# Kernel tuning notes

Measured on AMD Instinct MI355X. Metric: run time of the kernel, lower is better.

## Reference

```python
import jax, jax.numpy as jnp
import numpy as np

B, T, H, V, E = 128, 256, 512, 50000, 300
FORGET_BIAS = 1.0


def setup_inputs() -> dict:
    key = jax.random.key(0)
    ks = jax.random.split(key, 8)
    s = 0.05
    return {
        "x": jax.random.randint(ks[0], (B, T), 0, V, dtype=jnp.int64),
        "embedding": jax.random.normal(ks[1], (V, E), dtype=jnp.float32),
        "W0": jax.random.normal(ks[2], (E + H, 4 * H), dtype=jnp.float32) * s,
        "b0": jnp.zeros((4 * H,), dtype=jnp.float32),
        "W1": jax.random.normal(ks[3], (2 * H, 4 * H), dtype=jnp.float32) * s,
        "b1": jnp.zeros((4 * H,), dtype=jnp.float32),
        "Wd": jax.random.normal(ks[4], (H, 2), dtype=jnp.float32) * s,
        "bd": jnp.zeros((2,), dtype=jnp.float32),
    }


def _lstm_cell(x, c, h, W, b):
    # TF BasicLSTMCell: gates in i, j, f, o order; forget_bias added to f.
    g = jnp.dot(jnp.concatenate([x, h], axis=1), W) + b  # [B, 4H]
    i, j, f, o = jnp.split(g, 4, axis=1)
    c_new = c * jax.nn.sigmoid(f + FORGET_BIAS) + jax.nn.sigmoid(i) * jnp.tanh(j)
    h_new = jnp.tanh(c_new) * jax.nn.sigmoid(o)
    return c_new, h_new


def reference(x, embedding, W0, b0, W1, b1, Wd, bd):
    vecs = embedding[x]                      # [B, T, E] (frozen embedding lookup)
    vecs_t = jnp.transpose(vecs, (1, 0, 2))  # [T, B, E]

    def step(carry, xt):
        c0, h0, c1, h1 = carry
        c0, h0 = _lstm_cell(xt, c0, h0, W0, b0)
        c1, h1 = _lstm_cell(h0, c1, h1, W1, b1)
        return (c0, h0, c1, h1), None

    z = jnp.zeros((x.shape[0], W0.shape[1] // 4), dtype=embedding.dtype)
    (c0, h0, c1, h1), _ = jax.lax.scan(step, (z, z, z, z), vecs_t)
    logits = jnp.dot(h1, Wd) + bd            # [B, 2]
    return logits
```

## Files before the change

### kernel.cpp

```cpp
#include <hip/hip_runtime.h>

#define Tt 256

#define FLAGS_SHORTS 16384
#define H0OFF  16384
#define H1OFF  (H0OFF + 2*64*128*8)
#define HPAR   (64*128*8)

typedef _Float16 h8 __attribute__((ext_vector_type(8)));
typedef float    f4 __attribute__((ext_vector_type(4)));
typedef unsigned long long ull;
typedef unsigned short u16;

#define MFMA __builtin_amdgcn_mfma_f32_16x16x32_f16
#define LOSC (1.0f/1024.0f)

__device__ inline u16 h_bits(float f){ union{_Float16 h; u16 s;} u; u.h=(_Float16)f; return u.s; }
__device__ inline float bits_f(u16 s){ union{u16 s2; _Float16 h;} u; u.s2=s; return (float)u.h; }
__device__ inline float sigm(float x){ return 1.f/(1.f+expf(-x)); }

__device__ inline __amdgpu_buffer_rsrc_t make_rsrc(const void* base){
    return __builtin_amdgcn_make_buffer_rsrc((void*)base, (short)0,
                                             0xFFFFFFFFu,
                                             0x00020000);
}
__device__ inline h8 ldH(__amdgpu_buffer_rsrc_t rsrc, int u16idx){
    auto d = __builtin_amdgcn_raw_buffer_load_b128(rsrc, u16idx * 2, 0, 17 );
    h8 v; __builtin_memcpy(&v, &d, 16);
    return v;
}

__device__ inline void barrier_arrive(int* __restrict__ flags, int tid, int bid, int target) {
    __builtin_amdgcn_s_waitcnt(0);
    __syncthreads();
    if (tid == 0)
        __hip_atomic_store(flags + bid, target, __ATOMIC_RELAXED, __HIP_MEMORY_SCOPE_AGENT);
}
__device__ inline void barrier_wait(int* __restrict__ flags, int tid, int target) {
    if (tid < 256)
        while (__hip_atomic_load(flags + tid, __ATOMIC_RELAXED, __HIP_MEMORY_SCOPE_AGENT) < target)
            __builtin_amdgcn_s_sleep(4);
    __syncthreads();
}

struct X4 { f4 h0, l0, h1, l1; };

__global__ __launch_bounds__(1024, 1) void lstm_coop(
    const int* __restrict__ x, const float* __restrict__ emb,
    const float* __restrict__ W0, const float* __restrict__ b0,
    const float* __restrict__ W1, const float* __restrict__ b1,
    const float* __restrict__ Wd, const float* __restrict__ bd,
    float* __restrict__ out, u16* __restrict__ ws) {

    const int tid  = threadIdx.x;
    const int lane = tid & 63;
    const int wave = tid >> 6;
    const int mt   = wave & 3;
    const int g4   = wave >> 2;
    const int quad = lane >> 4;
    const int fm   = lane & 15;
    const int bid  = blockIdx.x;
    const int lyr  = bid & 1;
    const int inner= bid >> 1;
    const int bq   = inner >> 6;
    const int cg   = inner & 63;

    __shared__ u16   whi[128 * 32 * 8];
    __shared__ u16   wlo[128 * 32 * 8];
    __shared__ float csm[2][64 * 33];

    int* flags = (int*)ws;
    const __amdgpu_buffer_rsrc_t rsrc = make_rsrc(ws);

    if (lyr == 0) {
        for (int i = tid; i < 104 * 32 * 8; i += 1024) {
            int kg = i >> 8; int rem = i & 255; int n = rem >> 3; int j = rem & 7;
            int k = kg * 8 + j;
            int col = ((n >> 3) << 9) + (cg << 3) + (n & 7);
            float w = 0.f;
            if (k < 300) w = W0[k * 2048 + col];
            else if (k >= 320) w = W0[(k - 20) * 2048 + col];
            _Float16 wh = (_Float16)w;
            union{_Float16 h; u16 s;} uh; uh.h = wh;
            whi[i] = uh.s;
            wlo[i] = h_bits((w - (float)wh) * 1024.0f);
        }
    } else {
        for (int i = tid; i < 128 * 32 * 8; i += 1024) {
            int kg = i >> 8; int rem = i & 255; int n = rem >> 3; int j = rem & 7;
            int k = kg * 8 + j;
            int col = ((n >> 3) << 9) + (cg << 3) + (n & 7);
            float w = W1[k * 2048 + col];
            _Float16 wh = (_Float16)w;
            union{_Float16 h; u16 s;} uh; uh.h = wh;
            whi[i] = uh.s;
            wlo[i] = h_bits((w - (float)wh) * 1024.0f);
        }
    }

    if (tid < 256) {
        int row = bq * 64 + (tid >> 2);
        int c = (tid & 3) << 1;
        unsigned int* pz = (unsigned int*)(ws + (lyr ? H1OFF + 1 * HPAR : H0OFF + 0 * HPAR)
                                           + cg * 1024 + row * 8 + c);
        __hip_atomic_store(pz, 0u, __ATOMIC_RELAXED, __HIP_MEMORY_SCOPE_AGENT);
    }

    const int arow = bq * 64 + mt * 16 + fm;
    const int actm   = tid >> 3;
    const int acthc  = tid & 7;
    const int actrow = bq * 64 + actm;
    const int ca = (cg << 3) + acthc;

    const float bi = lyr ? b1[ca]        : b0[ca];
    const float bj = lyr ? b1[512 + ca]  : b0[512 + ca];
    const float bf = lyr ? b1[1024 + ca] : b0[1024 + ca];
    const float bo = lyr ? b1[1536 + ca] : b0[1536 + ca];

    float cs = 0.f;

    auto xgemm = [&](int pp) -> X4 {
        X4 a; a.h0 = (f4){0,0,0,0}; a.l0 = a.h0; a.h1 = a.h0; a.l1 = a.h0;
        int xi = x[arow * Tt + pp];
        xi = (xi < 0) ? 0 : ((xi >= 50000) ? 49999 : xi);
        const float* embrow = emb + (size_t)xi * 300;
#pragma unroll
        for (int ktl = 0; ktl < 3; ktl++) {
            int kt = ktl * 4 + g4;
            if (kt < 10) {
                int kbase = kt * 32 + quad * 8;
                h8 af;
                if (kt < 9) {
                    f4 u0 = *(const f4*)(embrow + kbase);
                    f4 u1 = *(const f4*)(embrow + kbase + 4);
#pragma unroll
                    for (int e = 0; e < 4; e++) { af[e] = (_Float16)u0[e]; af[4+e] = (_Float16)u1[e]; }
                } else {
#pragma unroll
                    for (int e = 0; e < 8; e++) { int kk = kbase + e; af[e] = (_Float16)((kk < 300) ? embrow[kk] : 0.f); }
                }
                int kb = (kt * 4 + quad) * 32;
                a.h0 = MFMA(af, *(const h8*)&whi[(kb + fm) * 8],      a.h0, 0,0,0);
                a.l0 = MFMA(af, *(const h8*)&wlo[(kb + fm) * 8],      a.l0, 0,0,0);
                a.h1 = MFMA(af, *(const h8*)&whi[(kb + 16 + fm) * 8], a.h1, 0,0,0);
                a.l1 = MFMA(af, *(const h8*)&wlo[(kb + 16 + fm) * 8], a.l1, 0,0,0);
            }
        }
        return a;
    };

    auto reduce_store = [&](const f4& aH0, const f4& aL0, const f4& aH1, const f4& aL1){
        if (g4 < 2) {
#pragma unroll
            for (int r = 0; r < 4; r++) {
                csm[g4][(mt * 16 + quad * 4 + r) * 33 + fm]      = aH0[r] + aL0[r] * LOSC;
                csm[g4][(mt * 16 + quad * 4 + r) * 33 + 16 + fm] = aH1[r] + aL1[r] * LOSC;
            }
        }
        __syncthreads();
        if (g4 >= 2) {
#pragma unroll
            for (int r = 0; r < 4; r++) {
                csm[g4 - 2][(mt * 16 + quad * 4 + r) * 33 + fm]      += aH0[r] + aL0[r] * LOSC;
                csm[g4 - 2][(mt * 16 + quad * 4 + r) * 33 + 16 + fm] += aH1[r] + aL1[r] * LOSC;
            }
        }
        __syncthreads();
    };

    X4 accx;
    barrier_arrive(flags, tid, bid, 1);
    if (lyr == 0) accx = xgemm(0);
    barrier_wait(flags, tid, 1);

    for (int p = 0; p <= Tt; ++p) {
        const int par = p & 1, wpar = 1 - par;

        if (lyr == 1) {
            if (p >= 1) {
                f4 aH0 = (f4){0,0,0,0}, aL0 = aH0, aH1 = aH0, aL1 = aH0;
                const int hpo = (g4 >= 2 ? H1OFF : H0OFF) + par * HPAR + arow * 8;
                const int ktbase = g4 * 8;
                const int ltbase = (g4 & 1) * 8;
                h8 af[8];
#pragma unroll
                for (int ktl = 0; ktl < 8; ktl++)
                    af[ktl] = ldH(rsrc, hpo + ((ltbase + ktl) * 4 + quad) * 1024);
#pragma unroll
                for (int ktl = 0; ktl < 8; ktl++) {
                    int kb = ((ktbase + ktl) * 4 + quad) * 32;
                    aH0 = MFMA(af[ktl], *(const h8*)&whi[(kb + fm) * 8],      aH0, 0,0,0);
                    aL0 = MFMA(af[ktl], *(const h8*)&wlo[(kb + fm) * 8],      aL0, 0,0,0);
                    aH1 = MFMA(af[ktl], *(const h8*)&whi[(kb + 16 + fm) * 8], aH1, 0,0,0);
                    aL1 = MFMA(af[ktl], *(const h8*)&wlo[(kb + 16 + fm) * 8], aL1, 0,0,0);
                }
                reduce_store(aH0, aL0, aH1, aL1);
                if (tid < 512) {
                    float gi = csm[0][actm * 33 + acthc]      + csm[1][actm * 33 + acthc]      + bi;
                    float gj = csm[0][actm * 33 + 8 + acthc]  + csm[1][actm * 33 + 8 + acthc]  + bj;
                    float gf = csm[0][actm * 33 + 16 + acthc] + csm[1][actm * 33 + 16 + acthc] + bf;
                    float go = csm[0][actm * 33 + 24 + acthc] + csm[1][actm * 33 + 24 + acthc] + bo;
                    cs = cs * sigm(gf + 1.f) + sigm(gi) * tanhf(gj);
                    float hv = tanhf(cs) * sigm(go);
                    u16 hb = h_bits(hv);
                    unsigned int pa = (unsigned int)hb | (((unsigned int)(u16)__shfl_xor((int)hb, 1, 64)) << 16);
                    if (!(acthc & 1)) {
                        u16* base = ws + H1OFF + wpar * HPAR + cg * 1024 + actrow * 8;
                        __hip_atomic_store((unsigned int*)(base + acthc), pa, __ATOMIC_RELAXED, __HIP_MEMORY_SCOPE_AGENT);
                    }
                }
            }
        } else {
            if (p < Tt) {
                f4 aH0 = accx.h0, aL0 = accx.l0, aH1 = accx.h1, aL1 = accx.l1;
                const int h0o = H0OFF + par * HPAR + arow * 8;
                h8 af[4];
#pragma unroll
                for (int ktl = 0; ktl < 4; ktl++) {
                    int kt = 10 + g4 * 4 + ktl;
                    af[ktl] = ldH(rsrc, h0o + ((kt - 10) * 4 + quad) * 1024);
                }
#pragma unroll
                for (int ktl = 0; ktl < 4; ktl++) {
                    int kt = 10 + g4 * 4 + ktl;
                    int kb = (kt * 4 + quad) * 32;
                    aH0 = MFMA(af[ktl], *(const h8*)&whi[(kb + fm) * 8],      aH0, 0,0,0);
                    aL0 = MFMA(af[ktl], *(const h8*)&wlo[(kb + fm) * 8],      aL0, 0,0,0);
                    aH1 = MFMA(af[ktl], *(const h8*)&whi[(kb + 16 + fm) * 8], aH1, 0,0,0);
                    aL1 = MFMA(af[ktl], *(const h8*)&wlo[(kb + 16 + fm) * 8], aL1, 0,0,0);
                }
                reduce_store(aH0, aL0, aH1, aL1);
                if (tid < 512) {
                    float gi = csm[0][actm * 33 + acthc]      + csm[1][actm * 33 + acthc]      + bi;
                    float gj = csm[0][actm * 33 + 8 + acthc]  + csm[1][actm * 33 + 8 + acthc]  + bj;
                    float gf = csm[0][actm * 33 + 16 + acthc] + csm[1][actm * 33 + 16 + acthc] + bf;
                    float go = csm[0][actm * 33 + 24 + acthc] + csm[1][actm * 33 + 24 + acthc] + bo;
                    cs = cs * sigm(gf + 1.f) + sigm(gi) * tanhf(gj);
                    float hv = tanhf(cs) * sigm(go);
                    u16 hb = h_bits(hv);
                    unsigned int pa = (unsigned int)hb | (((unsigned int)(u16)__shfl_xor((int)hb, 1, 64)) << 16);
                    if (!(acthc & 1)) {
                        u16* base = ws + H0OFF + wpar * HPAR + cg * 1024 + actrow * 8;
                        __hip_atomic_store((unsigned int*)(base + acthc), pa, __ATOMIC_RELAXED, __HIP_MEMORY_SCOPE_AGENT);
                    }
                }
            }
        }

        barrier_arrive(flags, tid, bid, p + 2);
        if (lyr == 0 && p + 1 < Tt) accx = xgemm(p + 1);
        barrier_wait(flags, tid, p + 2);
    }

    if (bid == 0 && tid < 256) {
        int b = tid >> 1, jj = tid & 1;
        float sum = bd[jj];
        const u16* hh = ws + H1OFF + 1 * HPAR;
        for (int g = 0; g < 64; g++) {
#pragma unroll
            for (int j4 = 0; j4 < 8; j4 += 4) {
                ull u = __hip_atomic_load((const ull*)(hh + (g * 128 + b) * 8 + j4),
                                          __ATOMIC_RELAXED, __HIP_MEMORY_SCOPE_AGENT);
#pragma unroll
                for (int e = 0; e < 4; e++)
                    sum += bits_f((u16)(u >> (16 * e))) * Wd[(g * 8 + j4 + e) * 2 + jj];
            }
        }
        out[b * 2 + jj] = sum;
    }
}

extern "C" void kernel_launch(void* const* d_in, const int* in_sizes, int n_in,
                              void* d_out, int out_size, void* d_ws, size_t ws_size,
                              hipStream_t stream) {
    const int*   x   = (const int*)d_in[0];
    const float* emb = (const float*)d_in[1];
    const float* W0  = (const float*)d_in[2];
    const float* b0  = (const float*)d_in[3];
    const float* W1  = (const float*)d_in[4];
    const float* b1  = (const float*)d_in[5];
    const float* Wd  = (const float*)d_in[6];
    const float* bd  = (const float*)d_in[7];
    float* out = (float*)d_out;
    u16* ws = (u16*)d_ws;

    void* args[] = { (void*)&x, (void*)&emb, (void*)&W0, (void*)&b0, (void*)&W1,
                     (void*)&b1, (void*)&Wd, (void*)&bd, (void*)&out, (void*)&ws };
    hipLaunchCooperativeKernel((void*)lstm_coop, dim3(256), dim3(1024), args, 0, stream);
}
```

Measured before the change: 1.705 ms.

## Stage hidden states into per-XCD copies with intra-XCD barrier

Each step, blocks on the same XCD cooperatively copy the current h0/h1 state from the global exchange buffer into a per-XCD staging area. They then synchronize with an XCD-local flag barrier and read their MFMA operands from that copy using cached (non-bypass) loads. The aim is to turn many coherent cross-die loads into a single copy per XCD, with later reads served from the local L2. This adds a second barrier and an extra global write/read round trip every timestep. Correctness depends on the rank assignment covering all 32 slices per XCD and on visibility ordering, which is weak here.

```diff
diff --git a/kernel.cpp b/kernel.cpp
--- a/kernel.cpp
+++ b/kernel.cpp
@@ -6,6 +6,8 @@
 #define H0OFF  16384
 #define H1OFF  (H0OFF + 2*64*128*8)
 #define HPAR   (64*128*8)
+#define AUXOFF (H1OFF + 2*64*128*8)
+#define STGOFF (AUXOFF + 4096)
 
 typedef _Float16 h8 __attribute__((ext_vector_type(8)));
 typedef float    f4 __attribute__((ext_vector_type(4)));
@@ -26,6 +28,11 @@
 }
 __device__ inline h8 ldH(__amdgpu_buffer_rsrc_t rsrc, int u16idx){
     auto d = __builtin_amdgcn_raw_buffer_load_b128(rsrc, u16idx * 2, 0, 17 );
+    h8 v; __builtin_memcpy(&v, &d, 16);
+    return v;
+}
+__device__ inline h8 ldG(__amdgpu_buffer_rsrc_t rsrc, int u16idx){
+    auto d = __builtin_amdgcn_raw_buffer_load_b128(rsrc, u16idx * 2, 0, 1 );
     h8 v; __builtin_memcpy(&v, &d, 16);
     return v;
 }
@@ -68,9 +75,17 @@
     __shared__ u16   whi[128 * 32 * 8];
     __shared__ u16   wlo[128 * 32 * 8];
     __shared__ float csm[2][64 * 33];
+    __shared__ int   srank;
 
     int* flags = (int*)ws;
+    int* aux   = (int*)(ws + AUXOFF);
     const __amdgpu_buffer_rsrc_t rsrc = make_rsrc(ws);
+
+    int xcd;
+    asm("s_getreg_b32 %0, hwreg(HW_REG_XCC_ID)" : "=s"(xcd));
+    xcd &= 7;
+    int* xf = aux + 8 + xcd * 32;
+    const int stb = STGOFF + xcd * 2 * HPAR;
 
     if (lyr == 0) {
         for (int i = tid; i < 104 * 32 * 8; i += 1024) {
@@ -98,6 +113,9 @@
         }
     }
 
+    if (tid < 8)
+        __hip_atomic_store(aux + tid, 0, __ATOMIC_RELAXED, __HIP_MEMORY_SCOPE_AGENT);
+
     if (tid < 256) {
         int row = bq * 64 + (tid >> 2);
         int c = (tid & 3) << 1;
@@ -173,19 +191,45 @@
     if (lyr == 0) accx = xgemm(0);
     barrier_wait(flags, tid, 1);
 
+    if (tid == 0) {
+        int r = __hip_atomic_fetch_add(aux + xcd, 1, __ATOMIC_RELAXED, __HIP_MEMORY_SCOPE_AGENT);
+        srank = r & 31;
+    }
+    __syncthreads();
+    const int rank = srank;
+
     for (int p = 0; p <= Tt; ++p) {
         const int par = p & 1, wpar = 1 - par;
+
+        {
+            const int pb = par * HPAR;
+            if (tid < 512) {
+                int plane = tid >> 8;
+                int t = tid & 255;
+                int off = rank * 2048 + t * 8;
+                h8 v = ldH(rsrc, (plane ? H1OFF : H0OFF) + pb + off);
+                *(h8*)(ws + stb + plane * HPAR + off) = v;
+            }
+            __builtin_amdgcn_s_waitcnt(0);
+            __syncthreads();
+            if (tid == 0)
+                __hip_atomic_store(xf + rank, p + 2, __ATOMIC_RELAXED, __HIP_MEMORY_SCOPE_AGENT);
+            if (tid < 32)
+                while (__hip_atomic_load(xf + tid, __ATOMIC_RELAXED, __HIP_MEMORY_SCOPE_AGENT) < p + 2)
+                    __builtin_amdgcn_s_sleep(1);
+            __syncthreads();
+        }
 
         if (lyr == 1) {
             if (p >= 1) {
                 f4 aH0 = (f4){0,0,0,0}, aL0 = aH0, aH1 = aH0, aL1 = aH0;
-                const int hpo = (g4 >= 2 ? H1OFF : H0OFF) + par * HPAR + arow * 8;
+                const int hpo = stb + (g4 >= 2 ? HPAR : 0) + arow * 8;
                 const int ktbase = g4 * 8;
                 const int ltbase = (g4 & 1) * 8;
                 h8 af[8];
 #pragma unroll
                 for (int ktl = 0; ktl < 8; ktl++)
-                    af[ktl] = ldH(rsrc, hpo + ((ltbase + ktl) * 4 + quad) * 1024);
+                    af[ktl] = ldG(rsrc, hpo + ((ltbase + ktl) * 4 + quad) * 1024);
 #pragma unroll
                 for (int ktl = 0; ktl < 8; ktl++) {
                     int kb = ((ktbase + ktl) * 4 + quad) * 32;
@@ -213,12 +257,12 @@
         } else {
             if (p < Tt) {
                 f4 aH0 = accx.h0, aL0 = accx.l0, aH1 = accx.h1, aL1 = accx.l1;
-                const int h0o = H0OFF + par * HPAR + arow * 8;
+                const int h0o = stb + arow * 8;
                 h8 af[4];
 #pragma unroll
                 for (int ktl = 0; ktl < 4; ktl++) {
                     int kt = 10 + g4 * 4 + ktl;
-                    af[ktl] = ldH(rsrc, h0o + ((kt - 10) * 4 + quad) * 1024);
+                    af[ktl] = ldG(rsrc, h0o + ((kt - 10) * 4 + quad) * 1024);
                 }
 #pragma unroll
                 for (int ktl = 0; ktl < 4; ktl++) {
```

New measurement: 2.319 ms. 36.0% more time.

## Replicate hidden-state exchange buffers per XCD and read the local copy

Applied to the files above, without the earlier changes.

Each block now writes its new h values to eight replicated copies of the hidden-state buffers, one per XCD. It reads from the copy indexed by its own XCC_ID hardware register. The goal is to make the per-step h reads hit the XCD-local L2 instead of crossing dies, which sits on the latency-bound recurrent critical path. The cost is eight times the store traffic and workspace use, plus an assumption that writes reach the other XCD copies before the barrier releases.

```diff
diff --git a/kernel.cpp b/kernel.cpp
--- a/kernel.cpp
+++ b/kernel.cpp
@@ -4,8 +4,8 @@
 
 #define FLAGS_SHORTS 16384
 #define H0OFF  16384
-#define H1OFF  (H0OFF + 2*64*128*8)
 #define HPAR   (64*128*8)
+#define HCOPY  (4*HPAR)
 
 typedef _Float16 h8 __attribute__((ext_vector_type(8)));
 typedef float    f4 __attribute__((ext_vector_type(4)));
@@ -72,6 +72,11 @@
     int* flags = (int*)ws;
     const __amdgpu_buffer_rsrc_t rsrc = make_rsrc(ws);
 
+    int xcd;
+    asm("s_getreg_b32 %0, hwreg(HW_REG_XCC_ID)" : "=s"(xcd));
+    xcd &= 7;
+    const int rb = H0OFF + xcd * HCOPY;
+
     if (lyr == 0) {
         for (int i = tid; i < 104 * 32 * 8; i += 1024) {
             int kg = i >> 8; int rem = i & 255; int n = rem >> 3; int j = rem & 7;
@@ -101,9 +106,12 @@
     if (tid < 256) {
         int row = bq * 64 + (tid >> 2);
         int c = (tid & 3) << 1;
-        unsigned int* pz = (unsigned int*)(ws + (lyr ? H1OFF + 1 * HPAR : H0OFF + 0 * HPAR)
-                                           + cg * 1024 + row * 8 + c);
-        __hip_atomic_store(pz, 0u, __ATOMIC_RELAXED, __HIP_MEMORY_SCOPE_AGENT);
+        int off = (lyr ? 2 * HPAR + 1 * HPAR : 0) + cg * 1024 + row * 8 + c;
+#pragma unroll
+        for (int cpy = 0; cpy < 8; cpy++) {
+            unsigned int* pz = (unsigned int*)(ws + H0OFF + cpy * HCOPY + off);
+            __hip_atomic_store(pz, 0u, __ATOMIC_RELAXED, __HIP_MEMORY_SCOPE_AGENT);
+        }
     }
 
     const int arow = bq * 64 + mt * 16 + fm;
@@ -168,6 +176,14 @@
         __syncthreads();
     };
 
+    auto store_h = [&](int lyroff, int wpar, unsigned int pa, int acthc_) {
+        int off = lyroff + wpar * HPAR + cg * 1024 + actrow * 8 + acthc_;
+#pragma unroll
+        for (int cpy = 0; cpy < 8; cpy++)
+            __hip_atomic_store((unsigned int*)(ws + H0OFF + cpy * HCOPY + off), pa,
+                               __ATOMIC_RELAXED, __HIP_MEMORY_SCOPE_AGENT);
+    };
+
     X4 accx;
     barrier_arrive(flags, tid, bid, 1);
     if (lyr == 0) accx = xgemm(0);
@@ -179,7 +195,7 @@
         if (lyr == 1) {
             if (p >= 1) {
                 f4 aH0 = (f4){0,0,0,0}, aL0 = aH0, aH1 = aH0, aL1 = aH0;
-                const int hpo = (g4 >= 2 ? H1OFF : H0OFF) + par * HPAR + arow * 8;
+                const int hpo = rb + (g4 >= 2 ? 2 * HPAR : 0) + par * HPAR + arow * 8;
                 const int ktbase = g4 * 8;
                 const int ltbase = (g4 & 1) * 8;
                 h8 af[8];
@@ -204,16 +220,13 @@
                     float hv = tanhf(cs) * sigm(go);
                     u16 hb = h_bits(hv);
                     unsigned int pa = (unsigned int)hb | (((unsigned int)(u16)__shfl_xor((int)hb, 1, 64)) << 16);
-                    if (!(acthc & 1)) {
-                        u16* base = ws + H1OFF + wpar * HPAR + cg * 1024 + actrow * 8;
-                        __hip_atomic_store((unsigned int*)(base + acthc), pa, __ATOMIC_RELAXED, __HIP_MEMORY_SCOPE_AGENT);
-                    }
+                    if (!(acthc & 1)) store_h(2 * HPAR, wpar, pa, acthc);
                 }
             }
         } else {
             if (p < Tt) {
                 f4 aH0 = accx.h0, aL0 = accx.l0, aH1 = accx.h1, aL1 = accx.l1;
-                const int h0o = H0OFF + par * HPAR + arow * 8;
+                const int h0o = rb + par * HPAR + arow * 8;
                 h8 af[4];
 #pragma unroll
                 for (int ktl = 0; ktl < 4; ktl++) {
@@ -239,10 +252,7 @@
                     float hv = tanhf(cs) * sigm(go);
                     u16 hb = h_bits(hv);
                     unsigned int pa = (unsigned int)hb | (((unsigned int)(u16)__shfl_xor((int)hb, 1, 64)) << 16);
-                    if (!(acthc & 1)) {
-                        u16* base = ws + H0OFF + wpar * HPAR + cg * 1024 + actrow * 8;
-                        __hip_atomic_store((unsigned int*)(base + acthc), pa, __ATOMIC_RELAXED, __HIP_MEMORY_SCOPE_AGENT);
-                    }
+                    if (!(acthc & 1)) store_h(0, wpar, pa, acthc);
                 }
             }
         }
@@ -255,7 +265,7 @@
     if (bid == 0 && tid < 256) {
         int b = tid >> 1, jj = tid & 1;
         float sum = bd[jj];
-        const u16* hh = ws + H1OFF + 1 * HPAR;
+        const u16* hh = ws + H0OFF + 2 * HPAR + 1 * HPAR;
         for (int g = 0; g < 64; g++) {
 #pragma unroll
             for (int j4 = 0; j4 < 8; j4 += 4) {
```

New measurement: 1.761 ms. 1.03x slower.
